# Performance work log

Hardware: AMD Instinct MI355X
Metric: run time of the kernel (lower is better)

## Reference

```python
import jax, jax.numpy as jnp
import numpy as np

WS = 8            # window_size
SHIFT = WS // 2   # shift_size


def _relative_position_index(ws):
    coords = np.stack(np.meshgrid(np.arange(ws), np.arange(ws), indexing='ij'))  # (2, ws, ws)
    coords = coords.reshape(2, -1)                        # (2, ws^2)
    rel = coords[:, :, None] - coords[:, None, :]          # (2, ws^2, ws^2)
    rel = rel.transpose(1, 2, 0)
    rel[:, :, 0] += ws - 1
    rel[:, :, 1] += ws - 1
    rel[:, :, 0] *= 2 * ws - 1
    return rel.sum(-1).astype(np.int32)                   # (ws^2, ws^2)


def _shift_mask(H, W, ws, shift):
    # Swin-style region-id mask for shifted windows -> bool (nh, nw, ws^2, ws^2)
    img = np.zeros((H, W), dtype=np.int32)
    cnt = 0
    sl = (slice(0, -ws), slice(-ws, -shift), slice(-shift, None))
    for hs in sl:
        for wsl in sl:
            img[hs, wsl] = cnt
            cnt += 1
    nh, nw = H // ws, W // ws
    win = img.reshape(nh, ws, nw, ws).transpose(0, 2, 1, 3).reshape(nh, nw, ws * ws)
    return win[:, :, :, None] != win[:, :, None, :]


def setup_inputs() -> dict:
    key = jax.random.key(0)
    ks = jax.random.split(key, 6)
    B, H, W, D, NHEAD = 8, 256, 256, 96, 6
    x = jax.random.normal(ks[0], (B, H, W, D), dtype=jnp.float32)
    w_qkv = jax.random.normal(ks[1], (D, 3 * D), dtype=jnp.float32) * 0.05
    b_qkv = jnp.zeros((3 * D,), dtype=jnp.float32)
    w_out = jax.random.normal(ks[2], (D, D), dtype=jnp.float32) * 0.05
    b_out = jnp.zeros((D,), dtype=jnp.float32)
    rpe_table = jax.random.normal(ks[3], ((2 * WS - 1) ** 2, NHEAD), dtype=jnp.float32) * 0.02
    rp_index = jnp.asarray(_relative_position_index(WS))
    mask = jnp.asarray(_shift_mask(H, W, WS, SHIFT))
    return {"x": x, "w_qkv": w_qkv, "b_qkv": b_qkv, "w_out": w_out,
            "b_out": b_out, "rpe_table": rpe_table, "rp_index": rp_index, "mask": mask}


def _partition(t, ws):
    # (B, h, H, W, dk) -> (B, h, nh, nw, ws*ws, dk)
    B, h, H, W, dk = t.shape
    nh, nw = H // ws, W // ws
    t = t.reshape(B, h, nh, ws, nw, ws, dk).transpose(0, 1, 2, 4, 3, 5, 6)
    return t.reshape(B, h, nh, nw, ws * ws, dk)


def _merge(t, ws):
    # inverse of _partition -> (B, h, H, W, dk)
    B, h, nh, nw, _, dk = t.shape
    t = t.reshape(B, h, nh, nw, ws, ws, dk).transpose(0, 1, 2, 4, 3, 5, 6)
    return t.reshape(B, h, nh * ws, nw * ws, dk)


def reference(x, w_qkv, b_qkv, w_out, b_out, rpe_table, rp_index, mask):
    B, H, W, D = x.shape
    n_head = rpe_table.shape[1]
    d_k = D // n_head
    scale = 1.0 / np.sqrt(d_k)
    ws2 = mask.shape[-1]
    ws = int(round(ws2 ** 0.5))
    shift = ws // 2

    qkv = (x @ w_qkv + b_qkv).reshape(B, H, W, 3, n_head, d_k)
    qkv = qkv.transpose(3, 0, 4, 1, 2, 5)          # (3, B, h, H, W, dk)
    q, k, v = qkv[0], qkv[1], qkv[2]

    # cyclic shift
    q = jnp.roll(q, (-shift, -shift), axis=(2, 3))
    k = jnp.roll(k, (-shift, -shift), axis=(2, 3))
    v = jnp.roll(v, (-shift, -shift), axis=(2, 3))

    q = _partition(q, ws)                          # (B, h, nh, nw, ws^2, dk)
    k = _partition(k, ws)
    v = _partition(v, ws)

    scores = jnp.einsum('bhijqd,bhijkd->bhijqk', q, k) * scale
    bias = rpe_table[rp_index]                     # (ws^2, ws^2, h)
    scores = scores + bias.transpose(2, 0, 1)[None, :, None, None]
    scores = jnp.where(mask[None, None], -1e9, scores)
    attn = jax.nn.softmax(scores, axis=-1)

    out = jnp.einsum('bhijqk,bhijkd->bhijqd', attn, v)
    out = _merge(out, ws)                          # (B, h, H, W, dk)
    out = jnp.roll(out, (shift, shift), axis=(2, 3))
    out = out.transpose(0, 2, 3, 1, 4).reshape(B, H, W, D)
    return out @ w_out + b_out
```

## Files before the change

kernel.cpp:

```cpp
#include <hip/hip_runtime.h>
#include <stdint.h>

#define HH    256
#define DD    96
#define NH    6
#define WSZ   8

typedef __bf16 bf16_t;
typedef bf16_t bf16x8 __attribute__((ext_vector_type(8)));
typedef short  s16x4  __attribute__((ext_vector_type(4)));
typedef float  f32x4  __attribute__((ext_vector_type(4)));

union U2  { bf16_t h[2]; uint32_t u; };
union Upk { uint32_t u[2]; s16x4 s; };

#define LOG2E 1.44269504088896f

static __device__ __forceinline__ uint32_t pack2(float a, float b) {
    U2 x; x.h[0] = (bf16_t)a; x.h[1] = (bf16_t)b; return x.u;
}

static __device__ __forceinline__ f32x4 mfma16(s16x4 a, s16x4 b, f32x4 c) {
#if __has_builtin(__builtin_amdgcn_mfma_f32_16x16x16bf16_1k)
    return __builtin_amdgcn_mfma_f32_16x16x16bf16_1k(a, b, c, 0, 0, 0);
#else
    f32x4 d;
    asm volatile("v_mfma_f32_16x16x16_bf16 %0, %1, %2, %3"
                 : "=v"(d) : "v"(a), "v"(b), "v"(c));
    return d;
#endif
}

static __device__ __forceinline__ float fast_exp2(float x) {
#if __has_builtin(__builtin_amdgcn_exp2f)
    return __builtin_amdgcn_exp2f(x);
#else
    return exp2f(x);
#endif
}

static __device__ __forceinline__ float fast_rcp(float x) {
#if __has_builtin(__builtin_amdgcn_rcpf)
    return __builtin_amdgcn_rcpf(x);
#else
    return 1.0f / x;
#endif
}

#define OFF_WQT_HI 0
#define OFF_WQT_LO 36864
#define OFF_WV_HI  73728
#define OFF_WV_LO  92160
#define OFF_WO_HI  110592
#define OFF_WO_LO  129024
#define OFF_RPE    147456

static __device__ __forceinline__ int swz(int row, int col) {
    return row * 128 + ((((col >> 3) ^ (row & 15)) & 15) << 3) + (col & 7);
}

__global__ __launch_bounds__(256)
void prep_kernel(const float* __restrict__ wqkv, const float* __restrict__ wout,
                 const float* __restrict__ rpe, char* __restrict__ ws)
{
    bf16_t* wqt_hi = (bf16_t*)(ws + OFF_WQT_HI);
    bf16_t* wqt_lo = (bf16_t*)(ws + OFF_WQT_LO);
    bf16_t* wv_hi  = (bf16_t*)(ws + OFF_WV_HI);
    bf16_t* wv_lo  = (bf16_t*)(ws + OFF_WV_LO);
    bf16_t* wo_hi  = (bf16_t*)(ws + OFF_WO_HI);
    bf16_t* wo_lo  = (bf16_t*)(ws + OFF_WO_LO);
    float*  rpe_b  = (float*)(ws + OFF_RPE);

    int idx = blockIdx.x * 256 + threadIdx.x;
    {
        int j = idx & 7, lane = (idx >> 3) & 63, frag = idx >> 9;
        int c = lane & 15, g = lane >> 4;
        if (idx < 18432) {
            int ks = frag % 3, r2 = frag / 3, wh = r2 % 6, t = r2 / 6;
            int k = ks * 32 + g * 8 + j;
            float v = wqkv[k * 288 + t * 96 + wh * 16 + c];
            bf16_t h = (bf16_t)v;
            wqt_hi[idx] = h;
            wqt_lo[idx] = (bf16_t)(v - (float)h);
        }
        if (idx < 9216) {
            int ks = frag % 3, wh = frag / 3;
            int k = ks * 32 + g * 8 + j;
            float v = wqkv[k * 288 + 192 + wh * 16 + c];
            bf16_t h = (bf16_t)v;
            wv_hi[idx] = h;
            wv_lo[idx] = (bf16_t)(v - (float)h);
            float v2 = wout[k * 96 + wh * 16 + c];
            bf16_t h2 = (bf16_t)v2;
            wo_hi[idx] = h2;
            wo_lo[idx] = (bf16_t)(v2 - (float)h2);
        }
    }
    if (idx < 24576) {
        int i = idx & 3, lane = (idx >> 2) & 63, kt = (idx >> 8) & 3,
            nt = (idx >> 10) & 3, h = idx >> 12;
        int c = lane & 15, g = lane >> 4;
        int k = kt * 16 + g * 4 + i, q = nt * 16 + c;
        int qr = q >> 3, qc = q & 7, kr = k >> 3, kc = k & 7;
        rpe_b[idx] = rpe[((qr - kr + 7) * 15 + (qc - kc + 7)) * NH + h] * LOG2E;
    }
}

#define ATTN_LOOP(EDGE_ON)                                                      \
    _Pragma("unroll")                                                           \
    for (int nt = 0; nt < 4; ++nt) {                                            \
        f32x4 stc[4];                                                           \
        _Pragma("unroll")                                                       \
        for (int kt = 0; kt < 4; ++kt) {                                        \
            const f32x4 rc = *(const f32x4*)&rpe_b[(((w * 4 + nt) * 4 + kt) << 8) + lane * 4]; \
            stc[kt] = mfma16(akb[kt], aqb[nt], rc);                             \
        }                                                                       \
        int rq = 0;                                                             \
        if (EDGE_ON) {                                                          \
            int q = nt * 16 + c, qr = q >> 3, qc = q & 7;                       \
            rq = (e_wi ? (qr >= 4 ? 2 : 1) : 0) * 3 + (e_wj ? (qc >= 4 ? 2 : 1) : 0); \
        }                                                                       \
        float sv[16];                                                           \
        float sum = 0.f;                                                        \
        _Pragma("unroll")                                                       \
        for (int kt = 0; kt < 4; ++kt)                                          \
            _Pragma("unroll")                                                   \
            for (int i = 0; i < 4; ++i) {                                       \
                float s = stc[kt][i];                                           \
                if (EDGE_ON && (rk[kt][i] != rq)) s = -1e9f;                    \
                s = fast_exp2(s);                                               \
                sv[kt * 4 + i] = s;                                             \
                sum += s;                                                       \
            }                                                                   \
        sum += __shfl_xor(sum, 16);                                             \
        sum += __shfl_xor(sum, 32);                                             \
        const float rinv = fast_rcp(sum);                                       \
        f32x4 oa = zf;                                                          \
        _Pragma("unroll")                                                       \
        for (int ks2 = 0; ks2 < 4; ++ks2) {                                     \
            Upk pb;                                                             \
            pb.u[0] = pack2(sv[ks2 * 4 + 0], sv[ks2 * 4 + 1]);                  \
            pb.u[1] = pack2(sv[ks2 * 4 + 2], sv[ks2 * 4 + 3]);                  \
            oa = mfma16(avb[ks2], pb.s, oa);                                    \
        }                                                                       \
        uint2 hv;                                                               \
        hv.x = pack2(oa[0] * rinv, oa[1] * rinv);                               \
        hv.y = pack2(oa[2] * rinv, oa[3] * rinv);                               \
        *(uint2*)&o_hi[swz(nt * 16 + c, w * 16 + 4 * g)] = hv;                  \
    }

__global__ __launch_bounds__(768, 4)
void swin_mfma(const float* __restrict__ x,
               const float* __restrict__ b_qkv,
               const float* __restrict__ b_out,
               const char*  __restrict__ ws,
               float* __restrict__ out)
{
    __shared__ char smem[32768];

    const int tid  = threadIdx.x;
    const int w2   = tid >> 6;
    const int wv   = (w2 >= 6) ? 1 : 0;
    const int w    = w2 - 6 * wv;
    const int lane = tid & 63;
    const int g    = lane >> 4;
    const int c    = lane & 15;
    const int tl   = tid - (wv << 8) - (wv << 7);

    bf16_t* xs_hi = (bf16_t*)(smem + (wv << 14));
    bf16_t* o_hi  = xs_hi;

    const bf16_t* wqt_hi = (const bf16_t*)(ws + OFF_WQT_HI);
    const bf16_t* wv_hi  = (const bf16_t*)(ws + OFF_WV_HI);
    const bf16_t* wv_lo  = (const bf16_t*)(ws + OFF_WV_LO);
    const bf16_t* wo_hi  = (const bf16_t*)(ws + OFF_WO_HI);
    const bf16_t* wo_lo  = (const bf16_t*)(ws + OFF_WO_LO);
    const float*  rpe_b  = (const float*)(ws + OFF_RPE);

    const int blk = blockIdx.x;
    const int b   = blk >> 9;
    const int wi  = (blk >> 4) & 31;
    const int wj  = ((blk & 15) << 1) + wv;

    const bf16x8 qh0 = *(const bf16x8*)&wqt_hi[(w * 3 + 0) * 512 + lane * 8];
    const bf16x8 kh0 = *(const bf16x8*)&wqt_hi[((6 + w) * 3 + 0) * 512 + lane * 8];
    const bf16x8 vh0 = *(const bf16x8*)&wv_hi[(w * 3 + 0) * 512 + lane * 8];
    const bf16x8 vl0 = *(const bf16x8*)&wv_lo[(w * 3 + 0) * 512 + lane * 8];

    uint32_t pix[4];
    #pragma unroll
    for (int t = 0; t < 4; ++t) {
        int p = t * 16 + c;
        int gh = (wi * WSZ + (p >> 3) + 4) & 255;
        int gw = (wj * WSZ + (p & 7) + 4) & 255;
        pix[t] = (((uint32_t)b * HH + gh) << 8) + gw;
    }

    const f32x4 zf = {0.f, 0.f, 0.f, 0.f};

    #pragma unroll
    for (int it = 0; it < 4; ++it) {
        int f4  = tl + it * 384;
        int row = f4 / 24, c4 = f4 - row * 24;
        int r = row >> 3, cl = row & 7;
        int gh = (wi * WSZ + r + 4) & 255;
        int gw = (wj * WSZ + cl + 4) & 255;
        const float4 v = *(const float4*)(x + (((size_t)b * HH + gh) * HH + gw) * DD + c4 * 4);
        uint2 hv;
        hv.x = pack2(v.x, v.y); hv.y = pack2(v.z, v.w);
        *(uint2*)&xs_hi[swz(row, c4 * 4)] = hv;
    }
    __syncthreads();

    f32x4 aq[4], akk[4], av[4];
    {
        const float4 bq4 = *(const float4*)&b_qkv[w * 16 + 4 * g];
        const float4 bk4 = *(const float4*)&b_qkv[96 + w * 16 + 4 * g];
        const float  bv  = b_qkv[192 + w * 16 + c];
        #pragma unroll
        for (int t4 = 0; t4 < 4; ++t4) {
            aq[t4]  = (f32x4){bq4.x, bq4.y, bq4.z, bq4.w};
            akk[t4] = (f32x4){bk4.x, bk4.y, bk4.z, bk4.w};
            av[t4]  = (f32x4){bv, bv, bv, bv};
        }
    }
    #pragma unroll
    for (int ks = 0; ks < 3; ++ks) {
        bf16x8 ah[4];
        #pragma unroll
        for (int mt = 0; mt < 4; ++mt) {
            int e = (mt * 16 + c) * 128 + (((ks * 4 + g) ^ c) << 3);
            ah[mt] = *(const bf16x8*)&xs_hi[e];
        }
        const bf16x8 qh = (ks == 0) ? qh0 : *(const bf16x8*)&wqt_hi[(w * 3 + ks) * 512 + lane * 8];
        const bf16x8 kh = (ks == 0) ? kh0 : *(const bf16x8*)&wqt_hi[((6 + w) * 3 + ks) * 512 + lane * 8];
        const bf16x8 vh = (ks == 0) ? vh0 : *(const bf16x8*)&wv_hi[(w * 3 + ks) * 512 + lane * 8];
        const bf16x8 vl = (ks == 0) ? vl0 : *(const bf16x8*)&wv_lo[(w * 3 + ks) * 512 + lane * 8];
        #pragma unroll
        for (int mt = 0; mt < 4; ++mt) {
            aq[mt]  = __builtin_amdgcn_mfma_f32_16x16x32_bf16(qh, ah[mt], aq[mt], 0, 0, 0);
            akk[mt] = __builtin_amdgcn_mfma_f32_16x16x32_bf16(kh, ah[mt], akk[mt], 0, 0, 0);
            av[mt]  = __builtin_amdgcn_mfma_f32_16x16x32_bf16(ah[mt], vh, av[mt], 0, 0, 0);
            av[mt]  = __builtin_amdgcn_mfma_f32_16x16x32_bf16(ah[mt], vl, av[mt], 0, 0, 0);
        }
    }
    __syncthreads();

    s16x4 aqb[4], akb[4], avb[4];
    #pragma unroll
    for (int t = 0; t < 4; ++t) {
        Upk uq, uk, uv;
        const float qs = 0.25f * LOG2E;
        uq.u[0] = pack2(aq[t][0] * qs, aq[t][1] * qs);
        uq.u[1] = pack2(aq[t][2] * qs, aq[t][3] * qs);
        uk.u[0] = pack2(akk[t][0], akk[t][1]);
        uk.u[1] = pack2(akk[t][2], akk[t][3]);
        uv.u[0] = pack2(av[t][0], av[t][1]);
        uv.u[1] = pack2(av[t][2], av[t][3]);
        aqb[t] = uq.s; akb[t] = uk.s; avb[t] = uv.s;
    }

    const int e_wi = (wi == 31), e_wj = (wj == 31);
    const bool edge = e_wi || e_wj;
    int rk[4][4];
    if (edge) {
        #pragma unroll
        for (int kt = 0; kt < 4; ++kt)
            #pragma unroll
            for (int i = 0; i < 4; ++i) {
                int k = kt * 16 + g * 4 + i;
                int kr = k >> 3, kc = k & 7;
                rk[kt][i] = (e_wi ? (kr >= 4 ? 2 : 1) : 0) * 3 + (e_wj ? (kc >= 4 ? 2 : 1) : 0);
            }
        ATTN_LOOP(1)
    } else {
        ATTN_LOOP(0)
    }
    __syncthreads();

    f32x4 acc3[4];
    {
        const float4 bo4 = *(const float4*)&b_out[w * 16 + 4 * g];
        #pragma unroll
        for (int nt = 0; nt < 4; ++nt)
            acc3[nt] = (f32x4){bo4.x, bo4.y, bo4.z, bo4.w};
    }
    #pragma unroll
    for (int ks = 0; ks < 3; ++ks) {
        bf16x8 oh[4];
        #pragma unroll
        for (int nt = 0; nt < 4; ++nt) {
            int e = (nt * 16 + c) * 128 + (((ks * 4 + g) ^ c) << 3);
            oh[nt] = *(const bf16x8*)&o_hi[e];
        }
        const bf16x8 bh = *(const bf16x8*)&wo_hi[(w * 3 + ks) * 512 + lane * 8];
        const bf16x8 bl = *(const bf16x8*)&wo_lo[(w * 3 + ks) * 512 + lane * 8];
        #pragma unroll
        for (int nt = 0; nt < 4; ++nt) {
            acc3[nt] = __builtin_amdgcn_mfma_f32_16x16x32_bf16(bh, oh[nt], acc3[nt], 0, 0, 0);
            acc3[nt] = __builtin_amdgcn_mfma_f32_16x16x32_bf16(bl, oh[nt], acc3[nt], 0, 0, 0);
        }
    }
    #pragma unroll
    for (int nt = 0; nt < 4; ++nt)
        *(f32x4*)(out + (size_t)pix[nt] * DD + w * 16 + 4 * g) = acc3[nt];
}

extern "C" void kernel_launch(void* const* d_in, const int* in_sizes, int n_in,
                              void* d_out, int out_size, void* d_ws, size_t ws_size,
                              hipStream_t stream) {
    const float* x    = (const float*)d_in[0];
    const float* wqkv = (const float*)d_in[1];
    const float* bqkv = (const float*)d_in[2];
    const float* wout = (const float*)d_in[3];
    const float* bout = (const float*)d_in[4];
    const float* rpe  = (const float*)d_in[5];
    float* out = (float*)d_out;
    char* ws = (char*)d_ws;

    const int B = in_sizes[0] / (HH * HH * DD);

    hipLaunchKernelGGL(prep_kernel, dim3(96), dim3(256), 0, stream, wqkv, wout, rpe, ws);
    hipLaunchKernelGGL(swin_mfma, dim3(B * 512), dim3(768), 0, stream,
                       x, bqkv, bout, (const char*)ws, out);
}
```

Baseline: 166.6 us.

## Drop bf16 hi/lo split for V and output weights, simplify x load, add setprio

Removes the low-order bf16 correction terms for the V projection and output projection weights, halving those MFMA counts and the weight loads. It also simplifies the x tile load indexing to hoist a division, and raises wave priority around the attention loop. The precision change lowers accuracy of V and output projections to plain bf16, which may risk tolerance.

```diff
diff --git a/kernel.cpp b/kernel.cpp
--- a/kernel.cpp
+++ b/kernel.cpp
@@ -47,13 +47,10 @@
 #endif
 }
 
-#define OFF_WQT_HI 0
-#define OFF_WQT_LO 36864
-#define OFF_WV_HI  73728
-#define OFF_WV_LO  92160
-#define OFF_WO_HI  110592
-#define OFF_WO_LO  129024
-#define OFF_RPE    147456
+#define OFF_WQT  0
+#define OFF_WV   36864
+#define OFF_WO   55296
+#define OFF_RPE  73728
 
 static __device__ __forceinline__ int swz(int row, int col) {
     return row * 128 + ((((col >> 3) ^ (row & 15)) & 15) << 3) + (col & 7);
@@ -63,13 +60,10 @@
 void prep_kernel(const float* __restrict__ wqkv, const float* __restrict__ wout,
                  const float* __restrict__ rpe, char* __restrict__ ws)
 {
-    bf16_t* wqt_hi = (bf16_t*)(ws + OFF_WQT_HI);
-    bf16_t* wqt_lo = (bf16_t*)(ws + OFF_WQT_LO);
-    bf16_t* wv_hi  = (bf16_t*)(ws + OFF_WV_HI);
-    bf16_t* wv_lo  = (bf16_t*)(ws + OFF_WV_LO);
-    bf16_t* wo_hi  = (bf16_t*)(ws + OFF_WO_HI);
-    bf16_t* wo_lo  = (bf16_t*)(ws + OFF_WO_LO);
-    float*  rpe_b  = (float*)(ws + OFF_RPE);
+    bf16_t* wqt = (bf16_t*)(ws + OFF_WQT);
+    bf16_t* wv  = (bf16_t*)(ws + OFF_WV);
+    bf16_t* wo  = (bf16_t*)(ws + OFF_WO);
+    float*  rpe_b = (float*)(ws + OFF_RPE);
 
     int idx = blockIdx.x * 256 + threadIdx.x;
     {
@@ -78,22 +72,13 @@
         if (idx < 18432) {
             int ks = frag % 3, r2 = frag / 3, wh = r2 % 6, t = r2 / 6;
             int k = ks * 32 + g * 8 + j;
-            float v = wqkv[k * 288 + t * 96 + wh * 16 + c];
-            bf16_t h = (bf16_t)v;
-            wqt_hi[idx] = h;
-            wqt_lo[idx] = (bf16_t)(v - (float)h);
+            wqt[idx] = (bf16_t)wqkv[k * 288 + t * 96 + wh * 16 + c];
         }
         if (idx < 9216) {
             int ks = frag % 3, wh = frag / 3;
             int k = ks * 32 + g * 8 + j;
-            float v = wqkv[k * 288 + 192 + wh * 16 + c];
-            bf16_t h = (bf16_t)v;
-            wv_hi[idx] = h;
-            wv_lo[idx] = (bf16_t)(v - (float)h);
-            float v2 = wout[k * 96 + wh * 16 + c];
-            bf16_t h2 = (bf16_t)v2;
-            wo_hi[idx] = h2;
-            wo_lo[idx] = (bf16_t)(v2 - (float)h2);
+            wv[idx] = (bf16_t)wqkv[k * 288 + 192 + wh * 16 + c];
+            wo[idx] = (bf16_t)wout[k * 96 + wh * 16 + c];
         }
     }
     if (idx < 24576) {
@@ -170,22 +155,19 @@
     bf16_t* xs_hi = (bf16_t*)(smem + (wv << 14));
     bf16_t* o_hi  = xs_hi;
 
-    const bf16_t* wqt_hi = (const bf16_t*)(ws + OFF_WQT_HI);
-    const bf16_t* wv_hi  = (const bf16_t*)(ws + OFF_WV_HI);
-    const bf16_t* wv_lo  = (const bf16_t*)(ws + OFF_WV_LO);
-    const bf16_t* wo_hi  = (const bf16_t*)(ws + OFF_WO_HI);
-    const bf16_t* wo_lo  = (const bf16_t*)(ws + OFF_WO_LO);
-    const float*  rpe_b  = (const float*)(ws + OFF_RPE);
+    const bf16_t* wqt   = (const bf16_t*)(ws + OFF_WQT);
+    const bf16_t* wvp   = (const bf16_t*)(ws + OFF_WV);
+    const bf16_t* wop   = (const bf16_t*)(ws + OFF_WO);
+    const float*  rpe_b = (const float*)(ws + OFF_RPE);
 
     const int blk = blockIdx.x;
     const int b   = blk >> 9;
     const int wi  = (blk >> 4) & 31;
     const int wj  = ((blk & 15) << 1) + wv;
 
-    const bf16x8 qh0 = *(const bf16x8*)&wqt_hi[(w * 3 + 0) * 512 + lane * 8];
-    const bf16x8 kh0 = *(const bf16x8*)&wqt_hi[((6 + w) * 3 + 0) * 512 + lane * 8];
-    const bf16x8 vh0 = *(const bf16x8*)&wv_hi[(w * 3 + 0) * 512 + lane * 8];
-    const bf16x8 vl0 = *(const bf16x8*)&wv_lo[(w * 3 + 0) * 512 + lane * 8];
+    const bf16x8 qh0 = *(const bf16x8*)&wqt[(w * 3 + 0) * 512 + lane * 8];
+    const bf16x8 kh0 = *(const bf16x8*)&wqt[((6 + w) * 3 + 0) * 512 + lane * 8];
+    const bf16x8 vh0 = *(const bf16x8*)&wvp[(w * 3 + 0) * 512 + lane * 8];
 
     uint32_t pix[4];
     #pragma unroll
@@ -198,17 +180,20 @@
 
     const f32x4 zf = {0.f, 0.f, 0.f, 0.f};
 
-    #pragma unroll
-    for (int it = 0; it < 4; ++it) {
-        int f4  = tl + it * 384;
-        int row = f4 / 24, c4 = f4 - row * 24;
-        int r = row >> 3, cl = row & 7;
-        int gh = (wi * WSZ + r + 4) & 255;
-        int gw = (wj * WSZ + cl + 4) & 255;
-        const float4 v = *(const float4*)(x + (((size_t)b * HH + gh) * HH + gw) * DD + c4 * 4);
-        uint2 hv;
-        hv.x = pack2(v.x, v.y); hv.y = pack2(v.z, v.w);
-        *(uint2*)&xs_hi[swz(row, c4 * 4)] = hv;
+    {
+        const int r0  = tl / 24;
+        const int c40 = tl - r0 * 24;
+        #pragma unroll
+        for (int it = 0; it < 4; ++it) {
+            int row = r0 + it * 16;
+            int r = row >> 3, cl = row & 7;
+            int gh = (wi * WSZ + r + 4) & 255;
+            int gw = (wj * WSZ + cl + 4) & 255;
+            const float4 v = *(const float4*)(x + (((size_t)b * HH + gh) * HH + gw) * DD + c40 * 4);
+            uint2 hv;
+            hv.x = pack2(v.x, v.y); hv.y = pack2(v.z, v.w);
+            *(uint2*)&xs_hi[swz(row, c40 * 4)] = hv;
+        }
     }
     __syncthreads();
 
@@ -232,16 +217,14 @@
             int e = (mt * 16 + c) * 128 + (((ks * 4 + g) ^ c) << 3);
             ah[mt] = *(const bf16x8*)&xs_hi[e];
         }
-        const bf16x8 qh = (ks == 0) ? qh0 : *(const bf16x8*)&wqt_hi[(w * 3 + ks) * 512 + lane * 8];
-        const bf16x8 kh = (ks == 0) ? kh0 : *(const bf16x8*)&wqt_hi[((6 + w) * 3 + ks) * 512 + lane * 8];
-        const bf16x8 vh = (ks == 0) ? vh0 : *(const bf16x8*)&wv_hi[(w * 3 + ks) * 512 + lane * 8];
-        const bf16x8 vl = (ks == 0) ? vl0 : *(const bf16x8*)&wv_lo[(w * 3 + ks) * 512 + lane * 8];
+        const bf16x8 qh = (ks == 0) ? qh0 : *(const bf16x8*)&wqt[(w * 3 + ks) * 512 + lane * 8];
+        const bf16x8 kh = (ks == 0) ? kh0 : *(const bf16x8*)&wqt[((6 + w) * 3 + ks) * 512 + lane * 8];
+        const bf16x8 vh = (ks == 0) ? vh0 : *(const bf16x8*)&wvp[(w * 3 + ks) * 512 + lane * 8];
         #pragma unroll
         for (int mt = 0; mt < 4; ++mt) {
             aq[mt]  = __builtin_amdgcn_mfma_f32_16x16x32_bf16(qh, ah[mt], aq[mt], 0, 0, 0);
             akk[mt] = __builtin_amdgcn_mfma_f32_16x16x32_bf16(kh, ah[mt], akk[mt], 0, 0, 0);
             av[mt]  = __builtin_amdgcn_mfma_f32_16x16x32_bf16(ah[mt], vh, av[mt], 0, 0, 0);
-            av[mt]  = __builtin_amdgcn_mfma_f32_16x16x32_bf16(ah[mt], vl, av[mt], 0, 0, 0);
         }
     }
     __syncthreads();
@@ -260,6 +243,7 @@
         aqb[t] = uq.s; akb[t] = uk.s; avb[t] = uv.s;
     }
 
+    __builtin_amdgcn_s_setprio(1);
     const int e_wi = (wi == 31), e_wj = (wj == 31);
     const bool edge = e_wi || e_wj;
     int rk[4][4];
@@ -276,6 +260,7 @@
     } else {
         ATTN_LOOP(0)
     }
+    __builtin_amdgcn_s_setprio(0);
     __syncthreads();
 
     f32x4 acc3[4];
@@ -293,13 +278,10 @@
             int e = (nt * 16 + c) * 128 + (((ks * 4 + g) ^ c) << 3);
             oh[nt] = *(const bf16x8*)&o_hi[e];
         }
-        const bf16x8 bh = *(const bf16x8*)&wo_hi[(w * 3 + ks) * 512 + lane * 8];
-        const bf16x8 bl = *(const bf16x8*)&wo_lo[(w * 3 + ks) * 512 + lane * 8];
-        #pragma unroll
-        for (int nt = 0; nt < 4; ++nt) {
+        const bf16x8 bh = *(const bf16x8*)&wop[(w * 3 + ks) * 512 + lane * 8];
+        #pragma unroll
+        for (int nt = 0; nt < 4; ++nt)
             acc3[nt] = __builtin_amdgcn_mfma_f32_16x16x32_bf16(bh, oh[nt], acc3[nt], 0, 0, 0);
-            acc3[nt] = __builtin_amdgcn_mfma_f32_16x16x32_bf16(bl, oh[nt], acc3[nt], 0, 0, 0);
-        }
     }
     #pragma unroll
     for (int nt = 0; nt < 4; ++nt)
```

New measurement: 158.8 us. 1.05x faster.
